# Kernel optimization log

Measured on AMD Instinct MI355X. Metric: run time of the kernel, lower is better.

The kernel has to match this reference:

```python
import jax, jax.numpy as jnp
import numpy as np
from jax.scipy.special import logsumexp

K, D, H, A = 8, 512, 512, 1024
S, T = 64, 128
B = S * T


def setup_inputs() -> dict:
    key = jax.random.key(0)
    k1, k2, k3, k4 = jax.random.split(key, 4)
    obs = jax.random.normal(k1, (B, D), dtype=jnp.float32)
    actions = jax.random.randint(k2, (B,), 0, A, dtype=jnp.int64)
    # uniform mixture prior (log(1/K)) => all components supported
    start_mixture_logprobs = jnp.full((S, K), jnp.log(1.0 / K), dtype=jnp.float32)
    W1 = jax.random.normal(k3, (K, D, H), dtype=jnp.float32) * 0.02
    b1 = jnp.zeros((K, H), dtype=jnp.float32)
    W2 = jax.random.normal(k4, (K, H, A), dtype=jnp.float32) * 0.02
    b2 = jnp.zeros((K, A), dtype=jnp.float32)
    return {"obs": obs, "actions": actions,
            "start_mixture_logprobs": start_mixture_logprobs,
            "W1": W1, "b1": b1, "W2": W2, "b2": b2, "seq_len": T}


def reference(obs, actions, start_mixture_logprobs, W1, b1, W2, b2, seq_len):
    num_seqs, num_comp = start_mixture_logprobs.shape
    batch = obs.shape[0]
    t_len = batch // num_seqs  # == seq_len
    num_out = W2.shape[-1]

    # per-component MLP on the full batch (all components supported)
    h = jax.nn.relu(jnp.einsum('bd,kdh->kbh', obs, W1) + b1[:, None, :])
    logits = jnp.einsum('kbh,kha->kba', h, W2) + b2[:, None, :]  # [K,B,A]
    component_logprobs = jax.nn.log_softmax(logits, axis=2)      # [K,B,A]

    # add time dimension: [B, K, A] -> [S, T, K, A]
    clp_t = component_logprobs.transpose(1, 0, 2).reshape(num_seqs, t_len, num_comp, num_out)
    act_t = actions.reshape(num_seqs, t_len)

    # gather logprob of taken action per component: [S, T, K]
    idx = jnp.broadcast_to(act_t[:, :, None, None], (num_seqs, t_len, num_comp, 1))
    action_logprobs = jnp.take_along_axis(clp_t, idx, axis=3)[..., 0]
    cum = jnp.cumsum(action_logprobs, axis=1)  # [S,T,K]

    # per-timestep posterior over mixture (shifted cumulative evidence)
    shift = jnp.concatenate([jnp.zeros((num_seqs, 1, num_comp), dtype=cum.dtype), cum[:, :-1]], axis=1)
    mix = jax.nn.log_softmax(start_mixture_logprobs[:, None, :] + shift, axis=2)  # [S,T,K]
    final_mixture_logprobs = jax.nn.log_softmax(start_mixture_logprobs + cum[:, -1], axis=1)

    # combine: logsumexp over components of component_logprobs + mixture logprob
    mix_flat = mix.reshape(batch, num_comp).T  # [K,B]
    model_out = logsumexp(component_logprobs + mix_flat[:, :, None], axis=0)  # [B,A]
    return model_out, final_mixture_logprobs
```

## Files before the change

kernel.cpp:

```cpp
#include <hip/hip_runtime.h>
#include <hip/hip_bf16.h>
#include <stdint.h>

#define KC   8
#define DIM  512
#define HID  512
#define ACTN 1024
#define NS   64
#define NT   128
#define NB   8192

typedef __attribute__((ext_vector_type(8))) short short8;
typedef __attribute__((ext_vector_type(8))) unsigned short ushort8;
typedef __attribute__((ext_vector_type(4))) float floatx4;
typedef __attribute__((ext_vector_type(4))) unsigned int uint4v;

__device__ inline float bf2f(unsigned short u) {
    return __uint_as_float(((unsigned int)u) << 16);
}
__device__ inline unsigned short f2bf(float x) {
    return __builtin_bit_cast(unsigned short, __float2bfloat16(x));
}

__global__ __launch_bounds__(256) void convert_bf16_kernel(
    const float* __restrict__ in, unsigned short* __restrict__ out, int n8)
{
    int i = blockIdx.x * 256 + threadIdx.x;
    if (i >= n8) return;
    const float* p = in + (size_t)i * 8;
    ushort8 u;
#pragma unroll
    for (int j = 0; j < 8; j++) u[j] = f2bf(p[j]);
    *(ushort8*)(out + (size_t)i * 8) = u;
}

__global__ __launch_bounds__(256) void transpose_bf16_kernel(
    const float* __restrict__ in, unsigned short* __restrict__ out, int R, int C)
{
    __shared__ float tile[32][33];
    int z = blockIdx.z;
    const float* src = in + (size_t)z * R * C;
    unsigned short* dst = out + (size_t)z * R * C;
    int c = blockIdx.x * 32 + threadIdx.x;
    int r0 = blockIdx.y * 32;
#pragma unroll
    for (int i = 0; i < 32; i += 8)
        tile[threadIdx.y + i][threadIdx.x] = src[(size_t)(r0 + threadIdx.y + i) * C + c];
    __syncthreads();
    int outr = blockIdx.x * 32 + threadIdx.y;
    int outc = r0 + threadIdx.x;
#pragma unroll
    for (int i = 0; i < 32; i += 8)
        dst[(size_t)(outr + i) * R + outc] = f2bf(tile[threadIdx.x][threadIdx.y + i]);
}

__global__ __launch_bounds__(256, 2) void gemm_bt_kernel(
    const unsigned short* __restrict__ Aall,
    const unsigned short* __restrict__ Btall,
    const float* __restrict__ biasall,
    unsigned short* __restrict__ Call,
    int M, int N, int Kd,
    long long strideA, long long strideBt, int strideBias, long long strideC,
    int do_relu)
{
    __shared__ __align__(16) unsigned short As[4][128][8];
    __shared__ __align__(16) unsigned short Bs[4][128][8];

    const int zb = blockIdx.z;
    const unsigned short* Ab  = Aall  + (size_t)zb * strideA;
    const unsigned short* Btb = Btall + (size_t)zb * strideBt;
    const float* bias = biasall + (size_t)zb * strideBias;
    unsigned short* Cb = Call + (size_t)zb * strideC;

    const int tid  = threadIdx.x;
    const int lane = tid & 63;
    const int wave = tid >> 6;
    const int wm = wave >> 1;
    const int wn = wave & 1;
    const int quad = lane >> 4;
    const int l16  = lane & 15;

    const int bm = blockIdx.x * 128;
    const int bn = blockIdx.y * 128;

    const int r0 = tid >> 2;
    const int c0 = tid & 3;

    floatx4 acc[4][4];
#pragma unroll
    for (int i = 0; i < 4; i++)
#pragma unroll
        for (int j = 0; j < 4; j++)
            acc[i][j] = (floatx4){0.f, 0.f, 0.f, 0.f};

    const unsigned short* aptr0 = Ab  + (size_t)(bm + r0)      * Kd + c0 * 8;
    const unsigned short* aptr1 = Ab  + (size_t)(bm + 64 + r0) * Kd + c0 * 8;
    const unsigned short* bptr0 = Btb + (size_t)(bn + r0)      * Kd + c0 * 8;
    const unsigned short* bptr1 = Btb + (size_t)(bn + 64 + r0) * Kd + c0 * 8;

    for (int k0 = 0; k0 < Kd; k0 += 32) {
        uint4v a0 = *(const uint4v*)(aptr0 + k0);
        uint4v a1 = *(const uint4v*)(aptr1 + k0);
        uint4v b0 = *(const uint4v*)(bptr0 + k0);
        uint4v b1 = *(const uint4v*)(bptr1 + k0);
        __syncthreads();
        *(uint4v*)&As[c0][r0][0]      = a0;
        *(uint4v*)&As[c0][64 + r0][0] = a1;
        *(uint4v*)&Bs[c0][r0][0]      = b0;
        *(uint4v*)&Bs[c0][64 + r0][0] = b1;
        __syncthreads();

        short8 af[4], bfr[4];
#pragma unroll
        for (int i = 0; i < 4; i++)
            af[i] = *(const short8*)&As[quad][wm * 64 + i * 16 + l16][0];
#pragma unroll
        for (int j = 0; j < 4; j++)
            bfr[j] = *(const short8*)&Bs[quad][wn * 64 + j * 16 + l16][0];
#pragma unroll
        for (int i = 0; i < 4; i++)
#pragma unroll
            for (int j = 0; j < 4; j++)
                acc[i][j] = __builtin_amdgcn_mfma_f32_16x16x32_bf16(
                    af[i], bfr[j], acc[i][j], 0, 0, 0);
    }

#pragma unroll
    for (int j = 0; j < 4; j++) {
        int col = bn + wn * 64 + j * 16 + l16;
        float bv = bias[col];
#pragma unroll
        for (int i = 0; i < 4; i++) {
            int rowb = bm + wm * 64 + i * 16 + quad * 4;
#pragma unroll
            for (int r = 0; r < 4; r++) {
                float v = acc[i][j][r] + bv;
                if (do_relu) v = fmaxf(v, 0.f);
                Cb[(size_t)(rowb + r) * N + col] = f2bf(v);
            }
        }
    }
}

__global__ __launch_bounds__(256) void row_reduce_kernel(
    const unsigned short* __restrict__ logits,
    const int* __restrict__ actions,
    float* __restrict__ lse,
    float* __restrict__ alp)
{
    int row  = blockIdx.x * 4 + (threadIdx.x >> 6);
    int lane = threadIdx.x & 63;
    int b = row & (NB - 1);
    const unsigned short* p = logits + (size_t)row * ACTN;
    ushort8 u0 = *(const ushort8*)(p + lane * 8);
    ushort8 u1 = *(const ushort8*)(p + 512 + lane * 8);
    float v[16];
#pragma unroll
    for (int j = 0; j < 8; j++) { v[j] = bf2f(u0[j]); v[8 + j] = bf2f(u1[j]); }
    float m = v[0];
#pragma unroll
    for (int j = 1; j < 16; j++) m = fmaxf(m, v[j]);
#pragma unroll
    for (int off = 32; off > 0; off >>= 1) m = fmaxf(m, __shfl_xor(m, off));
    float s = 0.f;
#pragma unroll
    for (int j = 0; j < 16; j++) s += __expf(v[j] - m);
#pragma unroll
    for (int off = 32; off > 0; off >>= 1) s += __shfl_xor(s, off);
    float l = m + __logf(s);

    int act = actions[b];
    int chunk = act >> 9;
    int within = act & 511;
    float av = 0.f;
    if (lane == (within >> 3)) av = v[chunk * 8 + (within & 7)];
#pragma unroll
    for (int off = 32; off > 0; off >>= 1) av += __shfl_xor(av, off);

    if (lane == 0) { lse[row] = l; alp[row] = av - l; }
}

__global__ __launch_bounds__(128) void mix_kernel(
    const float* __restrict__ alp,
    const float* __restrict__ start,
    const float* __restrict__ lse,
    float* __restrict__ w,
    float* __restrict__ fmix)
{
    __shared__ float buf[2][NT][9];
    int s = blockIdx.x, t = threadIdx.x;
    int b = s * NT + t;
    float a[KC];
#pragma unroll
    for (int k = 0; k < KC; k++) a[k] = alp[(size_t)k * NB + b];
#pragma unroll
    for (int k = 0; k < KC; k++) buf[0][t][k] = a[k];
    int p = 0;
    for (int off = 1; off < NT; off <<= 1) {
        __syncthreads();
#pragma unroll
        for (int k = 0; k < KC; k++) {
            float x = buf[p][t][k];
            if (t >= off) x += buf[p][t - off][k];
            buf[1 - p][t][k] = x;
        }
        p ^= 1;
    }
    __syncthreads();
    float st[KC], e[KC];
#pragma unroll
    for (int k = 0; k < KC; k++) st[k] = start[s * KC + k];
#pragma unroll
    for (int k = 0; k < KC; k++) e[k] = st[k] + buf[p][t][k] - a[k];
    float m = e[0];
#pragma unroll
    for (int k = 1; k < KC; k++) m = fmaxf(m, e[k]);
    float sum = 0.f;
#pragma unroll
    for (int k = 0; k < KC; k++) sum += __expf(e[k] - m);
    float l = m + __logf(sum);
#pragma unroll
    for (int k = 0; k < KC; k++)
        w[(size_t)k * NB + b] = (e[k] - l) - lse[(size_t)k * NB + b];

    if (t == NT - 1) {
        float f[KC];
#pragma unroll
        for (int k = 0; k < KC; k++) f[k] = st[k] + buf[p][t][k];
        float m2 = f[0];
#pragma unroll
        for (int k = 1; k < KC; k++) m2 = fmaxf(m2, f[k]);
        float s2 = 0.f;
#pragma unroll
        for (int k = 0; k < KC; k++) s2 += __expf(f[k] - m2);
        float l2 = m2 + __logf(s2);
#pragma unroll
        for (int k = 0; k < KC; k++) fmix[s * KC + k] = f[k] - l2;
    }
}

__global__ __launch_bounds__(128) void combine_kernel(
    const unsigned short* __restrict__ logits,
    const float* __restrict__ w,
    float* __restrict__ out)
{
    int b = blockIdx.x;
    int a0 = threadIdx.x * 8;
    float wv[KC];
#pragma unroll
    for (int k = 0; k < KC; k++) wv[k] = w[(size_t)k * NB + b];
    float x[KC][8];
#pragma unroll
    for (int k = 0; k < KC; k++) {
        ushort8 u = *(const ushort8*)(logits + ((size_t)k * NB + b) * ACTN + a0);
#pragma unroll
        for (int j = 0; j < 8; j++) x[k][j] = bf2f(u[j]) + wv[k];
    }
    float* op = out + (size_t)b * ACTN + a0;
#pragma unroll
    for (int j = 0; j < 8; j++) {
        float m = x[0][j];
#pragma unroll
        for (int k = 1; k < KC; k++) m = fmaxf(m, x[k][j]);
        float s = 0.f;
#pragma unroll
        for (int k = 0; k < KC; k++) s += __expf(x[k][j] - m);
        op[j] = m + __logf(s);
    }
}

extern "C" void kernel_launch(void* const* d_in, const int* in_sizes, int n_in,
                              void* d_out, int out_size, void* d_ws, size_t ws_size,
                              hipStream_t stream)
{
    const float* obs     = (const float*)d_in[0];
    const int*   actions = (const int*)d_in[1];
    const float* start   = (const float*)d_in[2];
    const float* W1      = (const float*)d_in[3];
    const float* b1      = (const float*)d_in[4];
    const float* W2      = (const float*)d_in[5];
    const float* b2      = (const float*)d_in[6];

    char* ws = (char*)d_ws;
    unsigned short* obs_bf = (unsigned short*)ws; ws += (size_t)NB * DIM * 2;
    unsigned short* W1t    = (unsigned short*)ws; ws += (size_t)KC * HID * DIM * 2;
    unsigned short* W2t    = (unsigned short*)ws; ws += (size_t)KC * ACTN * HID * 2;
    unsigned short* hbuf   = (unsigned short*)ws; ws += (size_t)KC * NB * HID * 2;
    unsigned short* logits = (unsigned short*)ws; ws += (size_t)KC * NB * ACTN * 2;
    float* lse  = (float*)ws; ws += (size_t)KC * NB * 4;
    float* alp  = (float*)ws; ws += (size_t)KC * NB * 4;
    float* wbuf = (float*)ws; ws += (size_t)KC * NB * 4;

    float* out  = (float*)d_out;
    float* fmix = out + (size_t)NB * ACTN;

    convert_bf16_kernel<<<(NB * DIM / 8 + 255) / 256, 256, 0, stream>>>(obs, obs_bf, NB * DIM / 8);
    transpose_bf16_kernel<<<dim3(HID / 32, DIM / 32, KC), dim3(32, 8), 0, stream>>>(W1, W1t, DIM, HID);
    transpose_bf16_kernel<<<dim3(ACTN / 32, HID / 32, KC), dim3(32, 8), 0, stream>>>(W2, W2t, HID, ACTN);

    gemm_bt_kernel<<<dim3(NB / 128, HID / 128, KC), 256, 0, stream>>>(
        obs_bf, W1t, b1, hbuf, NB, HID, DIM,
        0LL, (long long)HID * DIM, HID, (long long)NB * HID, 1);

    gemm_bt_kernel<<<dim3(NB / 128, ACTN / 128, KC), 256, 0, stream>>>(
        hbuf, W2t, b2, logits, NB, ACTN, HID,
        (long long)NB * HID, (long long)ACTN * HID, ACTN, (long long)NB * ACTN, 0);

    row_reduce_kernel<<<KC * NB / 4, 256, 0, stream>>>(logits, actions, lse, alp);

    mix_kernel<<<NS, NT, 0, stream>>>(alp, start, lse, wbuf, fmix);

    combine_kernel<<<NB, ACTN / 8, 0, stream>>>(logits, wbuf, out);
}
```

Measured before the change: 307.6 us.

## Fuse row logsumexp into GEMM epilogue and use direct global-to-LDS loads

```diff
diff --git a/kernel.cpp b/kernel.cpp
--- a/kernel.cpp
+++ b/kernel.cpp
@@ -9,6 +9,7 @@
 #define NS   64
 #define NT   128
 #define NB   8192
+#define PB   8
 
 typedef __attribute__((ext_vector_type(8))) short short8;
 typedef __attribute__((ext_vector_type(8))) unsigned short ushort8;
@@ -20,6 +21,13 @@
 }
 __device__ inline unsigned short f2bf(float x) {
     return __builtin_bit_cast(unsigned short, __float2bfloat16(x));
+}
+
+__device__ inline void gload_lds16(const unsigned short* g, unsigned short* l) {
+    __builtin_amdgcn_global_load_lds(
+        (const __attribute__((address_space(1))) unsigned int*)g,
+        (__attribute__((address_space(3))) unsigned int*)l,
+        16, 0, 0);
 }
 
 __global__ __launch_bounds__(256) void convert_bf16_kernel(
@@ -59,12 +67,15 @@
     const unsigned short* __restrict__ Btall,
     const float* __restrict__ biasall,
     unsigned short* __restrict__ Call,
+    const int* __restrict__ actions,
+    float* __restrict__ pmax, float* __restrict__ psum, float* __restrict__ palp,
     int M, int N, int Kd,
     long long strideA, long long strideBt, int strideBias, long long strideC,
-    int do_relu)
+    int do_relu, int do_lse)
 {
     __shared__ __align__(16) unsigned short As[4][128][8];
     __shared__ __align__(16) unsigned short Bs[4][128][8];
+    __shared__ __align__(16) unsigned short Cs[128][132];
 
     const int zb = blockIdx.z;
     const unsigned short* Ab  = Aall  + (size_t)zb * strideA;
@@ -83,9 +94,6 @@
     const int bm = blockIdx.x * 128;
     const int bn = blockIdx.y * 128;
 
-    const int r0 = tid >> 2;
-    const int c0 = tid & 3;
-
     floatx4 acc[4][4];
 #pragma unroll
     for (int i = 0; i < 4; i++)
@@ -93,21 +101,18 @@
         for (int j = 0; j < 4; j++)
             acc[i][j] = (floatx4){0.f, 0.f, 0.f, 0.f};
 
-    const unsigned short* aptr0 = Ab  + (size_t)(bm + r0)      * Kd + c0 * 8;
-    const unsigned short* aptr1 = Ab  + (size_t)(bm + 64 + r0) * Kd + c0 * 8;
-    const unsigned short* bptr0 = Btb + (size_t)(bn + r0)      * Kd + c0 * 8;
-    const unsigned short* bptr1 = Btb + (size_t)(bn + 64 + r0) * Kd + c0 * 8;
+    const unsigned short* gA = Ab  + (size_t)(bm + lane) * Kd + wave * 8;
+    const unsigned short* gB = Btb + (size_t)(bn + lane) * Kd + wave * 8;
+    unsigned short* lA = &As[wave][0][0];
+    unsigned short* lB = &Bs[wave][0][0];
+    const size_t rowskip = (size_t)64 * Kd;
 
     for (int k0 = 0; k0 < Kd; k0 += 32) {
-        uint4v a0 = *(const uint4v*)(aptr0 + k0);
-        uint4v a1 = *(const uint4v*)(aptr1 + k0);
-        uint4v b0 = *(const uint4v*)(bptr0 + k0);
-        uint4v b1 = *(const uint4v*)(bptr1 + k0);
         __syncthreads();
-        *(uint4v*)&As[c0][r0][0]      = a0;
-        *(uint4v*)&As[c0][64 + r0][0] = a1;
-        *(uint4v*)&Bs[c0][r0][0]      = b0;
-        *(uint4v*)&Bs[c0][64 + r0][0] = b1;
+        gload_lds16(gA + k0,           lA);
+        gload_lds16(gA + k0 + rowskip, lA + 64 * 8);
+        gload_lds16(gB + k0,           lB);
+        gload_lds16(gB + k0 + rowskip, lB + 64 * 8);
         __syncthreads();
 
         short8 af[4], bfr[4];
@@ -127,57 +132,80 @@
 
 #pragma unroll
     for (int j = 0; j < 4; j++) {
-        int col = bn + wn * 64 + j * 16 + l16;
-        float bv = bias[col];
+        int col = wn * 64 + j * 16 + l16;
+        float bv = bias[bn + col];
 #pragma unroll
         for (int i = 0; i < 4; i++) {
-            int rowb = bm + wm * 64 + i * 16 + quad * 4;
+            int row0 = wm * 64 + i * 16 + quad * 4;
 #pragma unroll
             for (int r = 0; r < 4; r++) {
                 float v = acc[i][j][r] + bv;
                 if (do_relu) v = fmaxf(v, 0.f);
-                Cb[(size_t)(rowb + r) * N + col] = f2bf(v);
+                Cs[row0 + r][col] = f2bf(v);
             }
         }
     }
-}
-
-__global__ __launch_bounds__(256) void row_reduce_kernel(
-    const unsigned short* __restrict__ logits,
-    const int* __restrict__ actions,
-    float* __restrict__ lse,
-    float* __restrict__ alp)
-{
-    int row  = blockIdx.x * 4 + (threadIdx.x >> 6);
-    int lane = threadIdx.x & 63;
-    int b = row & (NB - 1);
-    const unsigned short* p = logits + (size_t)row * ACTN;
-    ushort8 u0 = *(const ushort8*)(p + lane * 8);
-    ushort8 u1 = *(const ushort8*)(p + 512 + lane * 8);
-    float v[16];
-#pragma unroll
-    for (int j = 0; j < 8; j++) { v[j] = bf2f(u0[j]); v[8 + j] = bf2f(u1[j]); }
-    float m = v[0];
-#pragma unroll
-    for (int j = 1; j < 16; j++) m = fmaxf(m, v[j]);
-#pragma unroll
-    for (int off = 32; off > 0; off >>= 1) m = fmaxf(m, __shfl_xor(m, off));
+    __syncthreads();
+
+    const int row = tid >> 1;
+    const int ch  = (tid & 1) * 64;
+
+    float allm = 0.f;
+    if (do_lse) {
+        float m = -1e30f;
+#pragma unroll
+        for (int j = 0; j < 8; j++) {
+            ushort8 u = *(const ushort8*)&Cs[row][ch + 8 * j];
+#pragma unroll
+            for (int e = 0; e < 8; e++) m = fmaxf(m, bf2f(u[e]));
+        }
+        allm = fmaxf(m, __shfl_xor(m, 1));
+    }
+
+    unsigned short* crow = Cb + (size_t)(bm + row) * N + bn + ch;
     float s = 0.f;
 #pragma unroll
-    for (int j = 0; j < 16; j++) s += __expf(v[j] - m);
-#pragma unroll
-    for (int off = 32; off > 0; off >>= 1) s += __shfl_xor(s, off);
-    float l = m + __logf(s);
-
-    int act = actions[b];
-    int chunk = act >> 9;
-    int within = act & 511;
-    float av = 0.f;
-    if (lane == (within >> 3)) av = v[chunk * 8 + (within & 7)];
-#pragma unroll
-    for (int off = 32; off > 0; off >>= 1) av += __shfl_xor(av, off);
-
-    if (lane == 0) { lse[row] = l; alp[row] = av - l; }
+    for (int j = 0; j < 8; j++) {
+        ushort8 u = *(const ushort8*)&Cs[row][ch + 8 * j];
+        *(ushort8*)(crow + 8 * j) = u;
+        if (do_lse) {
+#pragma unroll
+            for (int e = 0; e < 8; e++) s += __expf(bf2f(u[e]) - allm);
+        }
+    }
+
+    if (do_lse) {
+        float stot = s + __shfl_xor(s, 1);
+        size_t kb = (size_t)zb * M + bm + row;
+        if ((tid & 1) == 0) {
+            pmax[kb * PB + blockIdx.y] = allm;
+            psum[kb * PB + blockIdx.y] = stot;
+        }
+        int act = actions[bm + row];
+        int rel = act - bn - ch;
+        if (rel >= 0 && rel < 64)
+            palp[kb] = bf2f(Cs[row][act - bn]);
+    }
+}
+
+__global__ __launch_bounds__(256) void lse_finish_kernel(
+    const float* __restrict__ pmax, const float* __restrict__ psum,
+    const float* __restrict__ palp,
+    float* __restrict__ lse, float* __restrict__ alp)
+{
+    int kb = blockIdx.x * 256 + threadIdx.x;
+    float m[PB];
+#pragma unroll
+    for (int p = 0; p < PB; p++) m[p] = pmax[(size_t)kb * PB + p];
+    float M = m[0];
+#pragma unroll
+    for (int p = 1; p < PB; p++) M = fmaxf(M, m[p]);
+    float S = 0.f;
+#pragma unroll
+    for (int p = 0; p < PB; p++) S += psum[(size_t)kb * PB + p] * __expf(m[p] - M);
+    float l = M + __logf(S);
+    lse[kb] = l;
+    alp[kb] = palp[kb] - l;
 }
 
 __global__ __launch_bounds__(128) void mix_kernel(
@@ -290,6 +318,9 @@
     float* lse  = (float*)ws; ws += (size_t)KC * NB * 4;
     float* alp  = (float*)ws; ws += (size_t)KC * NB * 4;
     float* wbuf = (float*)ws; ws += (size_t)KC * NB * 4;
+    float* pmax = (float*)ws; ws += (size_t)KC * NB * PB * 4;
+    float* psum = (float*)ws; ws += (size_t)KC * NB * PB * 4;
+    float* palp = (float*)ws; ws += (size_t)KC * NB * 4;
 
     float* out  = (float*)d_out;
     float* fmix = out + (size_t)NB * ACTN;
@@ -299,14 +330,14 @@
     transpose_bf16_kernel<<<dim3(ACTN / 32, HID / 32, KC), dim3(32, 8), 0, stream>>>(W2, W2t, HID, ACTN);
 
     gemm_bt_kernel<<<dim3(NB / 128, HID / 128, KC), 256, 0, stream>>>(
-        obs_bf, W1t, b1, hbuf, NB, HID, DIM,
-        0LL, (long long)HID * DIM, HID, (long long)NB * HID, 1);
+        obs_bf, W1t, b1, hbuf, actions, pmax, psum, palp,
+        NB, HID, DIM, 0LL, (long long)HID * DIM, HID, (long long)NB * HID, 1, 0);
 
     gemm_bt_kernel<<<dim3(NB / 128, ACTN / 128, KC), 256, 0, stream>>>(
-        hbuf, W2t, b2, logits, NB, ACTN, HID,
-        (long long)NB * HID, (long long)ACTN * HID, ACTN, (long long)NB * ACTN, 0);
-
-    row_reduce_kernel<<<KC * NB / 4, 256, 0, stream>>>(logits, actions, lse, alp);
+        hbuf, W2t, b2, logits, actions, pmax, psum, palp,
+        NB, ACTN, HID, (long long)NB * HID, (long long)ACTN * HID, ACTN, (long long)NB * ACTN, 0, 1);
+
+    lse_finish_kernel<<<KC * NB / 256, 256, 0, stream>>>(pmax, psum, palp, lse, alp);
 
     mix_kernel<<<NS, NT, 0, stream>>>(alp, start, lse, wbuf, fmix);
 
```

Measured after the change: 392.0 us. 27.4% more time.
